# Kernel tuning notes

Hardware: AMD Instinct MI355X
Metric: run time of the kernel (lower is better)

Reference implementation:

```python
import jax, jax.numpy as jnp
import numpy as np

MIDC = 256
HEADS = 8
HEADC = MIDC // HEADS
EPS = 1e-5


def _ln(x, gamma, beta):
    # LayerNorm over last dim (headc)
    mu = jnp.mean(x, axis=-1, keepdims=True)
    var = jnp.var(x, axis=-1, keepdims=True)
    return (x - mu) * jax.lax.rsqrt(var + EPS) * gamma + beta


def setup_inputs() -> dict:
    key = jax.random.key(0)
    ks = jax.random.split(key, 8)
    B, HW, C = 8, 4096, MIDC
    s = 1.0 / np.sqrt(C)
    return {
        "x": jax.random.normal(ks[0], (B, HW, C), jnp.float32),
        "w_qkv": jax.random.normal(ks[1], (C, 3 * C), jnp.float32) * s,
        "b_qkv": jnp.zeros((3 * C,), jnp.float32),
        "kln_g": jnp.ones((HEADC,), jnp.float32),
        "kln_b": jnp.zeros((HEADC,), jnp.float32),
        "vln_g": jnp.ones((HEADC,), jnp.float32),
        "vln_b": jnp.zeros((HEADC,), jnp.float32),
        "w1": jax.random.normal(ks[2], (C, C), jnp.float32) * s,
        "b1": jnp.zeros((C,), jnp.float32),
        "w2": jax.random.normal(ks[3], (C, C), jnp.float32) * s,
        "b2": jnp.zeros((C,), jnp.float32),
    }


def reference(x, w_qkv, b_qkv, kln_g, kln_b, vln_g, vln_b, w1, b1, w2, b2):
    B, HW, C = x.shape
    bias = x
    qkv = (x @ w_qkv + b_qkv).reshape(B, HW, HEADS, 3 * HEADC)
    qkv = qkv.transpose(0, 2, 1, 3)  # [B, h, HW, 3*headc]
    q, k, v = jnp.split(qkv, 3, axis=-1)  # each [B, h, HW, headc]
    k = _ln(k, kln_g, kln_b)
    v = _ln(v, vln_g, vln_b)
    # linear attention: (k^T v)/HW then q @ (.)
    kv = jnp.einsum('bhnd,bhne->bhde', k, v) / HW  # [B, h, headc, headc]
    out = jnp.einsum('bhnd,bhde->bhne', q, kv)     # [B, h, HW, headc]
    out = out.transpose(0, 2, 1, 3).reshape(B, HW, C)
    ret = out + bias
    # GELU MLP (torch nn.GELU default = exact erf form)
    h = jax.nn.gelu(ret @ w1 + b1, approximate=False)
    return h @ w2 + b2 + bias
```

## Files before the change

kernel.cpp:

```cpp
#include <hip/hip_runtime.h>
#include <hip/hip_bf16.h>
#include <math.h>

typedef _Float16 f16;
typedef _Float16 f16x4 __attribute__((ext_vector_type(4)));
typedef _Float16 f16x8 __attribute__((ext_vector_type(8)));
typedef float f32x4 __attribute__((ext_vector_type(4)));

#define MIDC 256
#define NHEADS 8
#define HEADC 32
#define HW_ 4096
#define BATCH 8
#define NTOK (BATCH*HW_)

__device__ __forceinline__ void gload_lds16(const void* g, void* lds){
    __builtin_amdgcn_global_load_lds(
        (const __attribute__((address_space(1))) unsigned int*)g,
        (__attribute__((address_space(3))) unsigned int*)lds, 16, 0, 0);
}

__global__ void k_f32_to_f16(const float* __restrict__ in, f16* __restrict__ out, int n){
    int i = (blockIdx.x*blockDim.x + threadIdx.x)*4;
    if (i < n) {
        float4 v = *reinterpret_cast<const float4*>(in + i);
        f16x4 o = { (f16)v.x, (f16)v.y, (f16)v.z, (f16)v.w };
        *reinterpret_cast<f16x4*>(out + i) = o;
    }
}

__global__ void k_transpose_f16(const float* __restrict__ in, f16* __restrict__ out, int R, int C){
    int idx = blockIdx.x*blockDim.x + threadIdx.x;
    if (idx < R*C) {
        int r = idx / C, c = idx % C;
        out[(size_t)c*R + r] = (f16)in[idx];
    }
}

__global__ void k_transpose_qkv(const float* __restrict__ in, f16* __restrict__ out){
    int idx = blockIdx.x*blockDim.x + threadIdx.x;
    int r = idx / 768, o = idx % 768;
    int h = o / 96, rr = o % 96, p = rr >> 5, d = o & 31;
    int n = (p << 8) + (h << 5) + d;
    out[(size_t)n*256 + r] = (f16)in[idx];
}

__global__ void k_permute_bias(const float* __restrict__ b, float* __restrict__ pb){
    int n = threadIdx.x;
    int p = n >> 8, h = (n & 255) >> 5, d = n & 31;
    pb[n] = b[h*96 + p*32 + d];
}

template<int MODE>
__global__ __launch_bounds__(256) void k_gemm(
    const f16* __restrict__ A, const f16* __restrict__ Bt,
    int K_,
    const float* __restrict__ bias,
    const float* __restrict__ kg_, const float* __restrict__ kb_,
    const float* __restrict__ vg_, const float* __restrict__ vb_,
    f16* __restrict__ oq, f16* __restrict__ ok, f16* __restrict__ ov,
    f16* __restrict__ oh,
    const float* __restrict__ resid, float* __restrict__ of)
{
    __shared__ __attribute__((aligned(16))) f16 As[128][32];
    __shared__ __attribute__((aligned(16))) f16 Bs[128][32];

    const int tid  = threadIdx.x;
    const int lane = tid & 63, wid = tid >> 6;
    const int m0 = blockIdx.y * 128, n0 = blockIdx.x * 128;
    const int wm = (wid >> 1) * 64, wn = (wid & 1) * 64;
    const int lr = lane & 15, kg = lane >> 4;

    f32x4 acc[4][4];
    f32x4 zero = {0.f,0.f,0.f,0.f};
    #pragma unroll
    for (int i=0;i<4;i++)
        #pragma unroll
        for (int j=0;j<4;j++) acc[i][j] = zero;

    const int srow = tid >> 2, scol = (tid & 3) * 8;
    const f16* gA = A  + (size_t)(m0 + srow)*K_ + scol;
    const f16* gB = Bt + (size_t)(n0 + srow)*K_ + scol;
    f16* asf = &As[0][0]; f16* bsf = &Bs[0][0];
    f16* as1 = asf + wid*512; f16* as2 = asf + 2048 + wid*512;
    f16* bs1 = bsf + wid*512; f16* bs2 = bsf + 2048 + wid*512;
    const size_t rstep = (size_t)64*K_;

    for (int kt = 0; kt < K_; kt += 32) {
        gload_lds16(gA + kt,          as1);
        gload_lds16(gA + kt + rstep,  as2);
        gload_lds16(gB + kt,          bs1);
        gload_lds16(gB + kt + rstep,  bs2);
        __syncthreads();
        f16x8 a[4], b[4];
        #pragma unroll
        for (int fr=0; fr<4; fr++) a[fr] = *reinterpret_cast<const f16x8*>(&As[wm + fr*16 + lr][kg*8]);
        #pragma unroll
        for (int fc=0; fc<4; fc++) b[fc] = *reinterpret_cast<const f16x8*>(&Bs[wn + fc*16 + lr][kg*8]);
        #pragma unroll
        for (int fr=0; fr<4; fr++)
            #pragma unroll
            for (int fc=0; fc<4; fc++)
                acc[fr][fc] = __builtin_amdgcn_mfma_f32_16x16x32_f16(a[fr], b[fc], acc[fr][fc], 0, 0, 0);
        __syncthreads();
    }

    if (MODE == 0) {
        int part = n0 >> 8;
        int nb = (n0 & 255) + wn;
        float g0=1.f, g1=1.f, be0=0.f, be1=0.f;
        if (part == 1){ g0 = kg_[lr]; g1 = kg_[lr+16]; be0 = kb_[lr]; be1 = kb_[lr+16]; }
        if (part == 2){ g0 = vg_[lr]; g1 = vg_[lr+16]; be0 = vb_[lr]; be1 = vb_[lr+16]; }
        f16* dst = (part == 0) ? oq : (part == 1 ? ok : ov);
        #pragma unroll
        for (int p2=0; p2<2; p2++){
            int colbase = nb + p2*32;
            int h = colbase >> 5;
            float bias0 = bias[n0 + wn + p2*32 + lr];
            float bias1 = bias[n0 + wn + p2*32 + 16 + lr];
            #pragma unroll
            for (int fr=0; fr<4; fr++)
            #pragma unroll
            for (int r=0; r<4; r++){
                float y0 = acc[fr][2*p2  ][r] + bias0;
                float y1 = acc[fr][2*p2+1][r] + bias1;
                int gm = m0 + wm + fr*16 + kg*4 + r;
                int b  = gm >> 12, n = gm & 4095;
                size_t base = (((size_t)(b*NHEADS + h))*HW_ + n)*HEADC;
                if (part == 0) {
                    dst[base + lr]      = (f16)y0;
                    dst[base + 16 + lr] = (f16)y1;
                } else {
                    float s = y0 + y1, s2 = y0*y0 + y1*y1;
                    #pragma unroll
                    for (int m=8; m>=1; m>>=1){ s += __shfl_xor(s, m); s2 += __shfl_xor(s2, m); }
                    float mu  = s * (1.0f/32.0f);
                    float var = s2 * (1.0f/32.0f) - mu*mu;
                    float rs  = rsqrtf(var + 1e-5f);
                    dst[base + lr]      = (f16)((y0 - mu)*rs*g0 + be0);
                    dst[base + 16 + lr] = (f16)((y1 - mu)*rs*g1 + be1);
                }
            }
        }
    } else {
        #pragma unroll
        for (int fr=0; fr<4; fr++)
        #pragma unroll
        for (int fc=0; fc<4; fc++)
        #pragma unroll
        for (int r=0; r<4; r++){
            int gm = m0 + wm + fr*16 + kg*4 + r;
            int gn = n0 + wn + fc*16 + lr;
            float v = acc[fr][fc][r] + bias[gn];
            if (MODE == 1) {
                float g = 0.5f * v * (1.0f + erff(v * 0.70710678f));
                oh[(size_t)gm*MIDC + gn] = (f16)g;
            } else {
                of[(size_t)gm*MIDC + gn] = v + resid[(size_t)gm*MIDC + gn];
            }
        }
    }
}

__global__ __launch_bounds__(256) void k_kv(const f16* __restrict__ kb, const f16* __restrict__ vb,
                                            float* __restrict__ kvpart){
    __shared__ __attribute__((aligned(16))) f16 ks[4][64][32];
    __shared__ __attribute__((aligned(16))) f16 vs[4][64][32];
    __shared__ __attribute__((aligned(16))) float red[4][32][32];
    const int bh = blockIdx.x, chunk = blockIdx.y;
    const int tid = threadIdx.x, lane = tid & 63, wid = tid >> 6;
    const int d0 = (lane >> 3) * 4, e0 = (lane & 7) * 4;
    const int tok0 = chunk*256 + wid*64;

    const f16* kg = kb + ((size_t)bh*HW_ + tok0)*HEADC;
    const f16* vg = vb + ((size_t)bh*HW_ + tok0)*HEADC;
    f16* ksw = &ks[wid][0][0]; f16* vsw = &vs[wid][0][0];
    #pragma unroll
    for (int i=0;i<4;i++){
        gload_lds16(kg + (size_t)(i*16 + (lane>>2))*HEADC + (lane&3)*8, ksw + i*512);
        gload_lds16(vg + (size_t)(i*16 + (lane>>2))*HEADC + (lane&3)*8, vsw + i*512);
    }
    __syncthreads();

    f32x4 acc[4];
    #pragma unroll
    for (int i=0;i<4;i++) acc[i] = (f32x4){0.f,0.f,0.f,0.f};
    #pragma unroll 4
    for (int t=0; t<64; t++){
        f16x4 kk = *reinterpret_cast<const f16x4*>(&ks[wid][t][d0]);
        f16x4 vv = *reinterpret_cast<const f16x4*>(&vs[wid][t][e0]);
        f32x4 vf = { (float)vv[0], (float)vv[1], (float)vv[2], (float)vv[3] };
        #pragma unroll
        for (int i=0;i<4;i++) acc[i] += (float)kk[i] * vf;
    }
    __syncthreads();
    #pragma unroll
    for (int i=0;i<4;i++) *reinterpret_cast<f32x4*>(&red[wid][d0+i][e0]) = acc[i];
    __syncthreads();
    int de0 = tid * 4;
    const float* rf = &red[0][0][0];
    f32x4 s = *reinterpret_cast<const f32x4*>(rf + de0);
    #pragma unroll
    for (int w=1; w<4; w++) s += *reinterpret_cast<const f32x4*>(rf + w*1024 + de0);
    *reinterpret_cast<f32x4*>(kvpart + ((size_t)bh*16 + chunk)*1024 + de0) = s;
}

__global__ void k_kvred(const float* __restrict__ kvpart, f16* __restrict__ kvT){
    int gid = blockIdx.x*blockDim.x + threadIdx.x;
    int bh = gid >> 10, de = gid & 1023;
    int d = de >> 5, e = de & 31;
    float s = 0.f;
    #pragma unroll
    for (int p=0; p<16; p++) s += kvpart[((size_t)bh*16 + p)*1024 + de];
    kvT[((size_t)bh << 10) + (e << 5) + d] = (f16)(s * (1.0f/4096.0f));
}

__global__ __launch_bounds__(256) void k_attn(const f16* __restrict__ qb, const f16* __restrict__ kvT,
                                              const float* __restrict__ x, f16* __restrict__ ret){
    const int bh = blockIdx.x, chunk = blockIdx.y;
    const int b = bh >> 3, h = bh & 7;
    const int tid = threadIdx.x, lane = tid & 63, wid = tid >> 6;
    const int lr = lane & 15, kg = lane >> 4;
    const int row0 = chunk*128 + wid*32;

    f32x4 acc[2][2];
    #pragma unroll
    for (int i=0;i<2;i++)
        #pragma unroll
        for (int j=0;j<2;j++) acc[i][j] = (f32x4){0.f,0.f,0.f,0.f};

    f16x8 a[2], bb[2];
    #pragma unroll
    for (int fr=0; fr<2; fr++)
        a[fr] = *reinterpret_cast<const f16x8*>(qb + ((size_t)bh*HW_ + row0 + fr*16 + lr)*HEADC + kg*8);
    #pragma unroll
    for (int fc=0; fc<2; fc++)
        bb[fc] = *reinterpret_cast<const f16x8*>(kvT + ((size_t)bh << 10) + (size_t)(fc*16 + lr)*32 + kg*8);
    #pragma unroll
    for (int fr=0; fr<2; fr++)
        #pragma unroll
        for (int fc=0; fc<2; fc++)
            acc[fr][fc] = __builtin_amdgcn_mfma_f32_16x16x32_f16(a[fr], bb[fc], acc[fr][fc], 0, 0, 0);

    #pragma unroll
    for (int fr=0; fr<2; fr++)
    #pragma unroll
    for (int fc=0; fc<2; fc++)
    #pragma unroll
    for (int r=0; r<4; r++){
        int n = row0 + fr*16 + kg*4 + r;
        int e = fc*16 + lr;
        size_t xi = ((size_t)b*HW_ + n)*MIDC + h*HEADC + e;
        ret[xi] = (f16)(acc[fr][fc][r] + x[xi]);
    }
}

extern "C" void kernel_launch(void* const* d_in, const int* in_sizes, int n_in,
                              void* d_out, int out_size, void* d_ws, size_t ws_size,
                              hipStream_t stream) {
    const float* x     = (const float*)d_in[0];
    const float* w_qkv = (const float*)d_in[1];
    const float* b_qkv = (const float*)d_in[2];
    const float* kln_g = (const float*)d_in[3];
    const float* kln_b = (const float*)d_in[4];
    const float* vln_g = (const float*)d_in[5];
    const float* vln_b = (const float*)d_in[6];
    const float* w1    = (const float*)d_in[7];
    const float* b1    = (const float*)d_in[8];
    const float* w2    = (const float*)d_in[9];
    const float* b2    = (const float*)d_in[10];
    float* out = (float*)d_out;

    char* ws = (char*)d_ws;
    size_t off = 0;
    auto alloc = [&](size_t bytes) -> void* {
        void* p = ws + off; off += (bytes + 255) & ~255ULL; return p;
    };
    const size_t TOKB = (size_t)NTOK*MIDC*sizeof(f16);
    f16* xb    = (f16*)alloc(TOKB);
    f16* wqkvT = (f16*)alloc(768*256*sizeof(f16));
    f16* w1T   = (f16*)alloc(256*256*sizeof(f16));
    f16* w2T   = (f16*)alloc(256*256*sizeof(f16));
    float* pb  = (float*)alloc(768*sizeof(float));
    f16* qb    = (f16*)alloc(TOKB);
    f16* kb    = (f16*)alloc(TOKB);
    f16* vb    = (f16*)alloc(TOKB);
    float* kvpart = (float*)alloc((size_t)64*16*1024*sizeof(float));
    f16* kvT   = (f16*)alloc((size_t)64*1024*sizeof(f16));
    f16* retb = xb;
    f16* hb   = qb;

    k_f32_to_f16<<<dim3((NTOK*MIDC)/4/256), 256, 0, stream>>>(x, xb, NTOK*MIDC);
    k_transpose_qkv<<<dim3((256*768)/256), 256, 0, stream>>>(w_qkv, wqkvT);
    k_permute_bias<<<dim3(1), 768, 0, stream>>>(b_qkv, pb);
    k_transpose_f16<<<dim3(256), 256, 0, stream>>>(w1, w1T, 256, 256);
    k_transpose_f16<<<dim3(256), 256, 0, stream>>>(w2, w2T, 256, 256);

    k_gemm<0><<<dim3(768/128, NTOK/128), 256, 0, stream>>>(
        xb, wqkvT, 256, pb, kln_g, kln_b, vln_g, vln_b,
        qb, kb, vb, nullptr, nullptr, nullptr);

    k_kv<<<dim3(64, HW_/256), 256, 0, stream>>>(kb, vb, kvpart);
    k_kvred<<<dim3(65536/256), 256, 0, stream>>>(kvpart, kvT);

    k_attn<<<dim3(64, HW_/128), 256, 0, stream>>>(qb, kvT, x, retb);

    k_gemm<1><<<dim3(256/128, NTOK/128), 256, 0, stream>>>(
        retb, w1T, 256, b1, nullptr, nullptr, nullptr, nullptr,
        nullptr, nullptr, nullptr, hb, nullptr, nullptr);

    k_gemm<2><<<dim3(256/128, NTOK/128), 256, 0, stream>>>(
        hb, w2T, 256, b2, nullptr, nullptr, nullptr, nullptr,
        nullptr, nullptr, nullptr, nullptr, x, out);
}
```

Before: 218.4 us.

## Double-buffer GEMM loads, stage epilogue through LDS, use fp16 residuals, merge prep kernels

Pipelines GEMM K-tiles with double-buffered LDS loads and routes the QKV/MLP1 epilogues through LDS so each thread writes contiguous 16-byte vectors, with per-thread LayerNorm. Residual reads in attention and the final GEMM use the fp16 copy of x instead of fp32 to cut memory traffic. The four weight/bias prep kernels are merged into one launch. The larger LDS footprint may reduce occupancy, and the fp16 residual adds rounding error to the output.

Result: faster. 211.8 us (-3.0%).

```diff
diff --git a/kernel.cpp b/kernel.cpp
--- a/kernel.cpp
+++ b/kernel.cpp
@@ -29,41 +29,43 @@
     }
 }
 
-__global__ void k_transpose_f16(const float* __restrict__ in, f16* __restrict__ out, int R, int C){
+__global__ void k_prep(const float* __restrict__ wqkv, const float* __restrict__ w1,
+                       const float* __restrict__ w2, const float* __restrict__ bq,
+                       f16* __restrict__ wqkvT, f16* __restrict__ w1T,
+                       f16* __restrict__ w2T, float* __restrict__ pb){
     int idx = blockIdx.x*blockDim.x + threadIdx.x;
-    if (idx < R*C) {
-        int r = idx / C, c = idx % C;
-        out[(size_t)c*R + r] = (f16)in[idx];
-    }
-}
-
-__global__ void k_transpose_qkv(const float* __restrict__ in, f16* __restrict__ out){
-    int idx = blockIdx.x*blockDim.x + threadIdx.x;
-    int r = idx / 768, o = idx % 768;
-    int h = o / 96, rr = o % 96, p = rr >> 5, d = o & 31;
-    int n = (p << 8) + (h << 5) + d;
-    out[(size_t)n*256 + r] = (f16)in[idx];
-}
-
-__global__ void k_permute_bias(const float* __restrict__ b, float* __restrict__ pb){
-    int n = threadIdx.x;
-    int p = n >> 8, h = (n & 255) >> 5, d = n & 31;
-    pb[n] = b[h*96 + p*32 + d];
+    if (idx < 196608){
+        int r = idx / 768, o = idx % 768;
+        int h = o / 96, rr = o % 96, p = rr >> 5, d = o & 31;
+        int n = (p << 8) + (h << 5) + d;
+        wqkvT[(size_t)n*256 + r] = (f16)wqkv[idx];
+    } else if (idx < 262144){
+        int i = idx - 196608; int r = i >> 8, c = i & 255;
+        w1T[(size_t)c*256 + r] = (f16)w1[i];
+    } else if (idx < 327680){
+        int i = idx - 262144; int r = i >> 8, c = i & 255;
+        w2T[(size_t)c*256 + r] = (f16)w2[i];
+    } else if (idx < 328448){
+        int n = idx - 327680;
+        int p = n >> 8, h = (n & 255) >> 5, d = n & 31;
+        pb[n] = bq[h*96 + p*32 + d];
+    }
 }
 
 template<int MODE>
 __global__ __launch_bounds__(256) void k_gemm(
     const f16* __restrict__ A, const f16* __restrict__ Bt,
-    int K_,
     const float* __restrict__ bias,
     const float* __restrict__ kg_, const float* __restrict__ kb_,
     const float* __restrict__ vg_, const float* __restrict__ vb_,
     f16* __restrict__ oq, f16* __restrict__ ok, f16* __restrict__ ov,
     f16* __restrict__ oh,
-    const float* __restrict__ resid, float* __restrict__ of)
+    const f16* __restrict__ residh, float* __restrict__ of)
 {
-    __shared__ __attribute__((aligned(16))) f16 As[128][32];
-    __shared__ __attribute__((aligned(16))) f16 Bs[128][32];
+    constexpr int K = 256;
+    __shared__ __attribute__((aligned(16))) char smem[(MODE==2) ? 32768 : 50176];
+    f16* const AsB[2] = { (f16*)(smem),        (f16*)(smem+16384) };
+    f16* const BsB[2] = { (f16*)(smem+8192),   (f16*)(smem+24576) };
 
     const int tid  = threadIdx.x;
     const int lane = tid & 63, wid = tid >> 6;
@@ -72,31 +74,38 @@
     const int lr = lane & 15, kg = lane >> 4;
 
     f32x4 acc[4][4];
-    f32x4 zero = {0.f,0.f,0.f,0.f};
     #pragma unroll
     for (int i=0;i<4;i++)
         #pragma unroll
-        for (int j=0;j<4;j++) acc[i][j] = zero;
+        for (int j=0;j<4;j++) acc[i][j] = (f32x4){0.f,0.f,0.f,0.f};
 
     const int srow = tid >> 2, scol = (tid & 3) * 8;
-    const f16* gA = A  + (size_t)(m0 + srow)*K_ + scol;
-    const f16* gB = Bt + (size_t)(n0 + srow)*K_ + scol;
-    f16* asf = &As[0][0]; f16* bsf = &Bs[0][0];
-    f16* as1 = asf + wid*512; f16* as2 = asf + 2048 + wid*512;
-    f16* bs1 = bsf + wid*512; f16* bs2 = bsf + 2048 + wid*512;
-    const size_t rstep = (size_t)64*K_;
-
-    for (int kt = 0; kt < K_; kt += 32) {
-        gload_lds16(gA + kt,          as1);
-        gload_lds16(gA + kt + rstep,  as2);
-        gload_lds16(gB + kt,          bs1);
-        gload_lds16(gB + kt + rstep,  bs2);
-        __syncthreads();
+    const f16* gA = A  + (size_t)(m0 + srow)*K + scol;
+    const f16* gB = Bt + (size_t)(n0 + srow)*K + scol;
+    const size_t rstep = (size_t)64*K;
+
+    auto STAGE = [&](int b, int kt){
+        f16* ab = AsB[b] + wid*512;
+        f16* bb = BsB[b] + wid*512;
+        gload_lds16(gA + kt,          ab);
+        gload_lds16(gA + kt + rstep,  ab + 2048);
+        gload_lds16(gB + kt,          bb);
+        gload_lds16(gB + kt + rstep,  bb + 2048);
+    };
+
+    STAGE(1, 0);
+    __syncthreads();
+
+    #pragma unroll
+    for (int t = 0; t < 8; ++t){
+        const f16* Ac = (t & 1) ? AsB[0] : AsB[1];
+        const f16* Bc = (t & 1) ? BsB[0] : BsB[1];
+        if (t < 7) STAGE((t & 1) ? 1 : 0, (t+1)*32);
         f16x8 a[4], b[4];
         #pragma unroll
-        for (int fr=0; fr<4; fr++) a[fr] = *reinterpret_cast<const f16x8*>(&As[wm + fr*16 + lr][kg*8]);
-        #pragma unroll
-        for (int fc=0; fc<4; fc++) b[fc] = *reinterpret_cast<const f16x8*>(&Bs[wn + fc*16 + lr][kg*8]);
+        for (int fr=0; fr<4; fr++) a[fr] = *reinterpret_cast<const f16x8*>(Ac + (wm + fr*16 + lr)*32 + kg*8);
+        #pragma unroll
+        for (int fc=0; fc<4; fc++) b[fc] = *reinterpret_cast<const f16x8*>(Bc + (wn + fc*16 + lr)*32 + kg*8);
         #pragma unroll
         for (int fr=0; fr<4; fr++)
             #pragma unroll
@@ -105,41 +114,79 @@
         __syncthreads();
     }
 
-    if (MODE == 0) {
-        int part = n0 >> 8;
-        int nb = (n0 & 255) + wn;
-        float g0=1.f, g1=1.f, be0=0.f, be1=0.f;
-        if (part == 1){ g0 = kg_[lr]; g1 = kg_[lr+16]; be0 = kb_[lr]; be1 = kb_[lr+16]; }
-        if (part == 2){ g0 = vg_[lr]; g1 = vg_[lr+16]; be0 = vb_[lr]; be1 = vb_[lr+16]; }
-        f16* dst = (part == 0) ? oq : (part == 1 ? ok : ov);
-        #pragma unroll
-        for (int p2=0; p2<2; p2++){
-            int colbase = nb + p2*32;
-            int h = colbase >> 5;
-            float bias0 = bias[n0 + wn + p2*32 + lr];
-            float bias1 = bias[n0 + wn + p2*32 + 16 + lr];
-            #pragma unroll
-            for (int fr=0; fr<4; fr++)
-            #pragma unroll
-            for (int r=0; r<4; r++){
-                float y0 = acc[fr][2*p2  ][r] + bias0;
-                float y1 = acc[fr][2*p2+1][r] + bias1;
-                int gm = m0 + wm + fr*16 + kg*4 + r;
-                int b  = gm >> 12, n = gm & 4095;
-                size_t base = (((size_t)(b*NHEADS + h))*HW_ + n)*HEADC;
-                if (part == 0) {
-                    dst[base + lr]      = (f16)y0;
-                    dst[base + 16 + lr] = (f16)y1;
+    if constexpr (MODE != 2){
+        f16* Cs = (f16*)(smem + 16384);
+        float bv[4];
+        #pragma unroll
+        for (int fc=0; fc<4; fc++) bv[fc] = bias[n0 + wn + fc*16 + lr];
+        #pragma unroll
+        for (int fr=0; fr<4; fr++)
+        #pragma unroll
+        for (int fc=0; fc<4; fc++)
+        #pragma unroll
+        for (int r=0; r<4; r++){
+            float v = acc[fr][fc][r] + bv[fc];
+            if constexpr (MODE == 1) v = 0.5f * v * (1.0f + erff(v * 0.70710678f));
+            Cs[(wm + fr*16 + kg*4 + r)*132 + (wn + fc*16 + lr)] = (f16)v;
+        }
+        __syncthreads();
+        #pragma unroll
+        for (int i=0;i<2;i++){
+            int c = tid + i*256;
+            int row = c >> 2, hc = c & 3;
+            const f16* src = Cs + row*132 + hc*32;
+            f16x8 d0 = *reinterpret_cast<const f16x8*>(src);
+            f16x8 d1 = *reinterpret_cast<const f16x8*>(src + 8);
+            f16x8 d2 = *reinterpret_cast<const f16x8*>(src + 16);
+            f16x8 d3 = *reinterpret_cast<const f16x8*>(src + 24);
+            if constexpr (MODE == 0){
+                int col0 = n0 + hc*32;
+                int part = col0 >> 8;
+                int h = (col0 & 255) >> 5;
+                int gm = m0 + row, b = gm >> 12, n = gm & 4095;
+                f16* dst = (part==0 ? oq : (part==1 ? ok : ov))
+                         + ((size_t)(b*NHEADS + h)*HW_ + n)*HEADC;
+                if (part == 0){
+                    *reinterpret_cast<f16x8*>(dst)      = d0;
+                    *reinterpret_cast<f16x8*>(dst + 8)  = d1;
+                    *reinterpret_cast<f16x8*>(dst + 16) = d2;
+                    *reinterpret_cast<f16x8*>(dst + 24) = d3;
                 } else {
-                    float s = y0 + y1, s2 = y0*y0 + y1*y1;
+                    float vals[32];
                     #pragma unroll
-                    for (int m=8; m>=1; m>>=1){ s += __shfl_xor(s, m); s2 += __shfl_xor(s2, m); }
+                    for (int j=0;j<8;j++){
+                        vals[j]    = (float)d0[j];
+                        vals[8+j]  = (float)d1[j];
+                        vals[16+j] = (float)d2[j];
+                        vals[24+j] = (float)d3[j];
+                    }
+                    float s = 0.f, s2 = 0.f;
+                    #pragma unroll
+                    for (int j=0;j<32;j++){ s += vals[j]; s2 = fmaf(vals[j], vals[j], s2); }
                     float mu  = s * (1.0f/32.0f);
                     float var = s2 * (1.0f/32.0f) - mu*mu;
                     float rs  = rsqrtf(var + 1e-5f);
-                    dst[base + lr]      = (f16)((y0 - mu)*rs*g0 + be0);
-                    dst[base + 16 + lr] = (f16)((y1 - mu)*rs*g1 + be1);
+                    const float* gp = (part==1) ? kg_ : vg_;
+                    const float* bp = (part==1) ? kb_ : vb_;
+                    f16x8 o0, o1, o2, o3;
+                    #pragma unroll
+                    for (int j=0;j<8;j++){
+                        o0[j] = (f16)((vals[j]    - mu)*rs*gp[j]    + bp[j]);
+                        o1[j] = (f16)((vals[8+j]  - mu)*rs*gp[8+j]  + bp[8+j]);
+                        o2[j] = (f16)((vals[16+j] - mu)*rs*gp[16+j] + bp[16+j]);
+                        o3[j] = (f16)((vals[24+j] - mu)*rs*gp[24+j] + bp[24+j]);
+                    }
+                    *reinterpret_cast<f16x8*>(dst)      = o0;
+                    *reinterpret_cast<f16x8*>(dst + 8)  = o1;
+                    *reinterpret_cast<f16x8*>(dst + 16) = o2;
+                    *reinterpret_cast<f16x8*>(dst + 24) = o3;
                 }
+            } else {
+                f16* dst = oh + (size_t)(m0 + row)*MIDC + n0 + hc*32;
+                *reinterpret_cast<f16x8*>(dst)      = d0;
+                *reinterpret_cast<f16x8*>(dst + 8)  = d1;
+                *reinterpret_cast<f16x8*>(dst + 16) = d2;
+                *reinterpret_cast<f16x8*>(dst + 24) = d3;
             }
         }
     } else {
@@ -151,13 +198,8 @@
         for (int r=0; r<4; r++){
             int gm = m0 + wm + fr*16 + kg*4 + r;
             int gn = n0 + wn + fc*16 + lr;
-            float v = acc[fr][fc][r] + bias[gn];
-            if (MODE == 1) {
-                float g = 0.5f * v * (1.0f + erff(v * 0.70710678f));
-                oh[(size_t)gm*MIDC + gn] = (f16)g;
-            } else {
-                of[(size_t)gm*MIDC + gn] = v + resid[(size_t)gm*MIDC + gn];
-            }
+            size_t xi = (size_t)gm*MIDC + gn;
+            of[xi] = acc[fr][fc][r] + bias[gn] + (float)residh[xi];
         }
     }
 }
@@ -216,7 +258,7 @@
 }
 
 __global__ __launch_bounds__(256) void k_attn(const f16* __restrict__ qb, const f16* __restrict__ kvT,
-                                              const float* __restrict__ x, f16* __restrict__ ret){
+                                              const f16* __restrict__ xb, f16* __restrict__ ret){
     const int bh = blockIdx.x, chunk = blockIdx.y;
     const int b = bh >> 3, h = bh & 7;
     const int tid = threadIdx.x, lane = tid & 63, wid = tid >> 6;
@@ -251,7 +293,7 @@
         int n = row0 + fr*16 + kg*4 + r;
         int e = fc*16 + lr;
         size_t xi = ((size_t)b*HW_ + n)*MIDC + h*HEADC + e;
-        ret[xi] = (f16)(acc[fr][fc][r] + x[xi]);
+        ret[xi] = (f16)(acc[fr][fc][r] + (float)xb[xi]);
     }
 }
 
@@ -287,29 +329,26 @@
     f16* vb    = (f16*)alloc(TOKB);
     float* kvpart = (float*)alloc((size_t)64*16*1024*sizeof(float));
     f16* kvT   = (f16*)alloc((size_t)64*1024*sizeof(f16));
-    f16* retb = xb;
-    f16* hb   = qb;
+    f16* retb = vb;
+    f16* hb   = kb;
 
     k_f32_to_f16<<<dim3((NTOK*MIDC)/4/256), 256, 0, stream>>>(x, xb, NTOK*MIDC);
-    k_transpose_qkv<<<dim3((256*768)/256), 256, 0, stream>>>(w_qkv, wqkvT);
-    k_permute_bias<<<dim3(1), 768, 0, stream>>>(b_qkv, pb);
-    k_transpose_f16<<<dim3(256), 256, 0, stream>>>(w1, w1T, 256, 256);
-    k_transpose_f16<<<dim3(256), 256, 0, stream>>>(w2, w2T, 256, 256);
+    k_prep<<<dim3((328448+255)/256), 256, 0, stream>>>(w_qkv, w1, w2, b_qkv, wqkvT, w1T, w2T, pb);
 
     k_gemm<0><<<dim3(768/128, NTOK/128), 256, 0, stream>>>(
-        xb, wqkvT, 256, pb, kln_g, kln_b, vln_g, vln_b,
+        xb, wqkvT, pb, kln_g, kln_b, vln_g, vln_b,
         qb, kb, vb, nullptr, nullptr, nullptr);
 
     k_kv<<<dim3(64, HW_/256), 256, 0, stream>>>(kb, vb, kvpart);
     k_kvred<<<dim3(65536/256), 256, 0, stream>>>(kvpart, kvT);
 
-    k_attn<<<dim3(64, HW_/128), 256, 0, stream>>>(qb, kvT, x, retb);
+    k_attn<<<dim3(64, HW_/128), 256, 0, stream>>>(qb, kvT, xb, retb);
 
     k_gemm<1><<<dim3(256/128, NTOK/128), 256, 0, stream>>>(
-        retb, w1T, 256, b1, nullptr, nullptr, nullptr, nullptr,
+        retb, w1T, b1, nullptr, nullptr, nullptr, nullptr,
         nullptr, nullptr, nullptr, hb, nullptr, nullptr);
 
     k_gemm<2><<<dim3(256/128, NTOK/128), 256, 0, stream>>>(
-        hb, w2T, 256, b2, nullptr, nullptr, nullptr, nullptr,
-        nullptr, nullptr, nullptr, nullptr, x, out);
-}
+        hb, w2T, b2, nullptr, nullptr, nullptr, nullptr,
+        nullptr, nullptr, nullptr, nullptr, xb, out);
+}
```
